# Performance work log

Measured on AMD Instinct MI355X. Metric: run time of the kernel, lower is better.

The kernel has to match this reference:

```python
import jax, jax.numpy as jnp
import numpy as np

EPS = 1e-8
SIM_THRESHOLD = 0.5


def _conv(x, src, dst, W, b):
    # Gather per-edge endpoint features: x_j = source, x_i = target (PyG default flow)
    x_j = x[src]
    x_i = x[dst]
    # Cosine similarity per edge
    dot = jnp.sum(x_i * x_j, axis=1)
    denom = jnp.maximum(jnp.linalg.norm(x_i, axis=1) * jnp.linalg.norm(x_j, axis=1), EPS)
    sim = dot / denom
    mask = (sim > SIM_THRESHOLD).astype(x.dtype)[:, None]
    msg = x_j * mask
    # Scatter-add aggregate into target nodes
    agg = jax.ops.segment_sum(msg, dst, num_segments=x.shape[0])
    # update: Linear
    return agg @ W.T + b


def setup_inputs() -> dict:
    key = jax.random.key(0)
    k1, k2, k3, k4, k5 = jax.random.split(key, 5)
    N, E, D_IN, D_HID, D_OUT = 50000, 800000, 128, 256, 64
    x = jax.random.normal(k1, (N, D_IN), dtype=jnp.float32)
    edge_index = jax.random.randint(k2, (2, E), 0, N, dtype=jnp.int64)
    # Xavier-uniform linear weights, zero-ish bias
    lim1 = float(np.sqrt(6.0 / (D_IN + D_HID)))
    lim2 = float(np.sqrt(6.0 / (D_HID + D_OUT)))
    W1 = jax.random.uniform(k3, (D_HID, D_IN), minval=-lim1, maxval=lim1, dtype=jnp.float32)
    b1 = jnp.zeros((D_HID,), dtype=jnp.float32)
    W2 = jax.random.uniform(k4, (D_OUT, D_HID), minval=-lim2, maxval=lim2, dtype=jnp.float32)
    b2 = jnp.zeros((D_OUT,), dtype=jnp.float32)
    return {"x": x, "edge_index": edge_index, "W1": W1, "b1": b1, "W2": W2, "b2": b2}


def reference(x, edge_index, W1, b1, W2, b2):
    N = x.shape[0]
    # add self-loops
    loops = jnp.arange(N, dtype=edge_index.dtype)
    src = jnp.concatenate([edge_index[0], loops])
    dst = jnp.concatenate([edge_index[1], loops])
    h = _conv(x, src, dst, W1, b1)
    h = jax.nn.relu(h)  # dropout is identity in eval mode
    out = _conv(h, src, dst, W2, b2)
    return jax.nn.log_softmax(out, axis=-1)
```

## Files before the change

kernel.cpp:

```cpp
#include <hip/hip_runtime.h>
#include <math.h>

#define EPS 1e-8f
#define NB_SORT 256

#if defined(__has_builtin)
#if __has_builtin(__builtin_amdgcn_sdot4)
#define HAVE_SDOT4 1
#endif
#endif

typedef __attribute__((ext_vector_type(8))) short bf16x8;
typedef __attribute__((ext_vector_type(4))) float f32x4;

__device__ __forceinline__ int sdot4i(int a, int b, int c) {
#ifdef HAVE_SDOT4
  return __builtin_amdgcn_sdot4(a, b, c, false);
#else
  return c + ((int)(signed char)(a)) * ((int)(signed char)(b)) +
         ((int)(signed char)(a >> 8)) * ((int)(signed char)(b >> 8)) +
         ((int)(signed char)(a >> 16)) * ((int)(signed char)(b >> 16)) +
         (a >> 24) * (b >> 24);
#endif
}

__device__ __forceinline__ float wave_reduce_sum(float v) {
#pragma unroll
  for (int off = 32; off > 0; off >>= 1)
    v += __shfl_xor(v, off, 64);
  return v;
}

__device__ __forceinline__ float wave_reduce_max(float v) {
#pragma unroll
  for (int off = 32; off > 0; off >>= 1)
    v = fmaxf(v, __shfl_xor(v, off, 64));
  return v;
}

__device__ __forceinline__ float dot4(float4 a, float4 b) {
  return a.x * b.x + a.y * b.y + a.z * b.z + a.w * b.w;
}

__device__ __forceinline__ int clampq(float q) {
  int i = (int)rintf(q);
  return i < -127 ? -127 : (i > 127 ? 127 : i);
}

__device__ __forceinline__ void split_bf16(float x, unsigned int& hi,
                                           unsigned int& lo) {
  unsigned int u = __float_as_uint(x);
  hi = u >> 16;
  float hf = __uint_as_float(u & 0xFFFF0000u);
  float r = x - hf;
  lo = __float_as_uint(r) >> 16;
}

__global__ __launch_bounds__(256) void hist_coarse(const int* __restrict__ dst,
                                                   int* __restrict__ hist_blk,
                                                   int E, int nbuck) {
  __shared__ int lh[1024];
  int t = threadIdx.x, blk = blockIdx.x;
  for (int i = t; i < nbuck; i += 256) lh[i] = 0;
  __syncthreads();
  int ch = (E + NB_SORT - 1) / NB_SORT;
  int lo = blk * ch, hi = min(E, lo + ch);
  for (int e = lo + t; e < hi; e += 256) atomicAdd(&lh[dst[e] >> 6], 1);
  __syncthreads();
  for (int i = t; i < nbuck; i += 256) hist_blk[i * NB_SORT + blk] = lh[i];
}

__global__ __launch_bounds__(256) void scan_local(int* __restrict__ hist,
                                                  int* __restrict__ bsum,
                                                  int nb) {
  __shared__ int tsum[256];
  int t = threadIdx.x;
  int base = blockIdx.x * 1024 + t * 4;
  int v0 = 0, v1 = 0, v2 = 0, v3 = 0;
  if (base + 3 < nb) {
    int4 q = *(const int4*)&hist[base];
    v0 = q.x; v1 = q.y; v2 = q.z; v3 = q.w;
  } else {
    if (base + 0 < nb) v0 = hist[base + 0];
    if (base + 1 < nb) v1 = hist[base + 1];
    if (base + 2 < nb) v2 = hist[base + 2];
  }
  tsum[t] = v0 + v1 + v2 + v3;
  __syncthreads();
  for (int off = 1; off < 256; off <<= 1) {
    int u = 0;
    if (t >= off) u = tsum[t - off];
    __syncthreads();
    if (t >= off) tsum[t] += u;
    __syncthreads();
  }
  int excl = (t == 0) ? 0 : tsum[t - 1];
  int e0 = excl, e1 = excl + v0, e2 = e1 + v1, e3 = e2 + v2;
  if (base + 3 < nb) {
    *(int4*)&hist[base] = make_int4(e0, e1, e2, e3);
  } else {
    if (base + 0 < nb) hist[base + 0] = e0;
    if (base + 1 < nb) hist[base + 1] = e1;
    if (base + 2 < nb) hist[base + 2] = e2;
  }
  if (t == 255) bsum[blockIdx.x] = tsum[255];
}

__global__ __launch_bounds__(256) void scan_bsum(int* __restrict__ bsum,
                                                 int nblk) {
  __shared__ int sh[256];
  int t = threadIdx.x;
  sh[t] = (t < nblk) ? bsum[t] : 0;
  __syncthreads();
  for (int off = 1; off < 256; off <<= 1) {
    int u = 0;
    if (t >= off) u = sh[t - off];
    __syncthreads();
    if (t >= off) sh[t] += u;
    __syncthreads();
  }
  if (t < nblk) bsum[t] = (t == 0) ? 0 : sh[t - 1];
}

__global__ __launch_bounds__(256) void add_bsum(int* __restrict__ hist,
                                                const int* __restrict__ bsum,
                                                int nb) {
  int i = blockIdx.x * blockDim.x + threadIdx.x;
  if (i < nb) hist[i] += bsum[i >> 10];
}

__global__ __launch_bounds__(256) void scatter_coarse(
    const int* __restrict__ src, const int* __restrict__ dst,
    const int* __restrict__ S, int2* __restrict__ epair, int E, int nbuck) {
  __shared__ int lb[1024];
  int t = threadIdx.x, blk = blockIdx.x;
  for (int i = t; i < nbuck; i += 256) lb[i] = S[i * NB_SORT + blk];
  __syncthreads();
  int ch = (E + NB_SORT - 1) / NB_SORT;
  int lo = blk * ch, hi = min(E, lo + ch);
  for (int e = lo + t; e < hi; e += 256) {
    int d = dst[e];
    int pos = atomicAdd(&lb[d >> 6], 1);
    epair[pos] = make_int2(src[e], d);
  }
}

__global__ __launch_bounds__(256) void fine_sort(
    const int2* __restrict__ epair, const int* __restrict__ S,
    int2* __restrict__ spair, int E, int nbuck) {
  __shared__ int fh[64];
  __shared__ int cur[64];
  int b = blockIdx.x, t = threadIdx.x;
  int bstart = S[b * NB_SORT];
  int bend = (b + 1 < nbuck) ? S[(b + 1) * NB_SORT] : E;
  if (t < 64) fh[t] = 0;
  __syncthreads();
  for (int e = bstart + t; e < bend; e += 256)
    atomicAdd(&fh[epair[e].y & 63], 1);
  __syncthreads();
  if (t < 64) {
    int v = fh[t];
    int incl = v;
#pragma unroll
    for (int off = 1; off < 64; off <<= 1) {
      int u = __shfl_up(incl, off, 64);
      if (t >= off) incl += u;
    }
    cur[t] = incl - v;
  }
  __syncthreads();
  for (int e = bstart + t; e < bend; e += 256) {
    int2 p = epair[e];
    int pos = atomicAdd(&cur[p.y & 63], 1);
    spair[bstart + pos] = p;
  }
}

__global__ __launch_bounds__(256) void prep_x(const float* __restrict__ x,
                                              signed char* __restrict__ qx,
                                              float4* __restrict__ nprop,
                                              float* __restrict__ agg,
                                              int N) {
  int node = (int)((blockIdx.x * blockDim.x + threadIdx.x) >> 6);
  int lane = threadIdx.x & 63;
  if (node >= N) return;
  float2 v = *(const float2*)(x + (size_t)node * 128 + lane * 2);
  float ax = fabsf(v.x), ay = fabsf(v.y);
  float mx = wave_reduce_max(fmaxf(ax, ay));
  float l1 = wave_reduce_sum(ax + ay);
  float ss = wave_reduce_sum(v.x * v.x + v.y * v.y);
  float s = mx * (1.0f / 127.0f);
  float inv = (mx > 0.f) ? 127.0f / mx : 0.f;
  int q0 = clampq(v.x * inv), q1 = clampq(v.y * inv);
  unsigned short w = (unsigned short)((q0 & 0xff) | ((q1 & 0xff) << 8));
  ((unsigned short*)(qx + (size_t)node * 128))[lane] = w;
  float l1q = s * wave_reduce_sum((float)(abs(q0) + abs(q1)));
  bool sp = ss > 0.5f * fmaxf(ss, EPS);
  *(float2*)(agg + (size_t)node * 128 + lane * 2) =
      sp ? v : make_float2(0.f, 0.f);
  if (lane == 0)
    nprop[node] = make_float4(sqrtf(ss), s, fmaxf(l1, l1q), 0.f);
}

__global__ __launch_bounds__(256) void prep_h(const float* __restrict__ h,
                                              signed char* __restrict__ qh,
                                              float4* __restrict__ nprop,
                                              float* __restrict__ agg,
                                              int N) {
  int node = (int)((blockIdx.x * blockDim.x + threadIdx.x) >> 6);
  int lane = threadIdx.x & 63;
  if (node >= N) return;
  float4 v = *(const float4*)(h + (size_t)node * 256 + lane * 4);
  float ax = fabsf(v.x), ay = fabsf(v.y), az = fabsf(v.z), aw = fabsf(v.w);
  float mx = wave_reduce_max(fmaxf(fmaxf(ax, ay), fmaxf(az, aw)));
  float l1 = wave_reduce_sum(ax + ay + az + aw);
  float ss = wave_reduce_sum(dot4(v, v));
  float s = mx * (1.0f / 127.0f);
  float inv = (mx > 0.f) ? 127.0f / mx : 0.f;
  int q0 = clampq(v.x * inv), q1 = clampq(v.y * inv);
  int q2 = clampq(v.z * inv), q3 = clampq(v.w * inv);
  int w = (q0 & 0xff) | ((q1 & 0xff) << 8) | ((q2 & 0xff) << 16) | (q3 << 24);
  ((int*)(qh + (size_t)node * 256))[lane] = w;
  float l1q = s * wave_reduce_sum((float)(abs(q0) + abs(q1) + abs(q2) + abs(q3)));
  bool sp = ss > 0.5f * fmaxf(ss, EPS);
  *(float4*)(agg + (size_t)node * 256 + lane * 4) =
      sp ? v : make_float4(0.f, 0.f, 0.f, 0.f);
  if (lane == 0)
    nprop[node] = make_float4(sqrtf(ss), s, fmaxf(l1, l1q), 0.f);
}

template <int D>
__global__ __launch_bounds__(256) void conv_coop(
    const float* __restrict__ xf, const signed char* __restrict__ qt,
    const float4* __restrict__ nprop, const int2* __restrict__ spair,
    float* __restrict__ agg, int E) {
  constexpr int G = D / 16;
  constexpr int EPW = 64 / G;
  constexpr int V = D / 64;
  const int tid = threadIdx.x;
  const int lane = tid & 63;
  const int wv = tid >> 6;
  const int g = lane & (G - 1);
  const int sub = lane / G;
  const int e = (blockIdx.x * 4 + wv) * EPW + sub;
  const bool valid = e < E;
  int2 p = spair[valid ? e : (E - 1)];
  const int s = p.x, d = p.y;
  float4 nps = nprop[s];
  float4 npd = nprop[d];
  int id = 0;
  {
    int4 a = *(const int4*)(qt + (size_t)s * D + g * 16);
    int4 bq = *(const int4*)(qt + (size_t)d * D + g * 16);
    id = sdot4i(a.x, bq.x, id);
    id = sdot4i(a.y, bq.y, id);
    id = sdot4i(a.z, bq.z, id);
    id = sdot4i(a.w, bq.w, id);
  }
#pragma unroll
  for (int off = G / 2; off > 0; off >>= 1) id += __shfl_xor(id, off, 64);
  float denom = fmaxf(nps.x * npd.x, EPS);
  float thr = 0.5f * denom;
  float approx = (nps.y * npd.y) * (float)id;
  float m = 0.5002f * (nps.y * npd.z + npd.y * nps.z) + 2e-6f * denom + 1e-7f;
  bool maybe = valid && (approx > thr - m);
  bool defp = maybe && (approx - m > thr);
  bool amb = maybe && !defp;
  unsigned long long defmask = __ballot(defp && g == 0);
  unsigned long long ambmask = __ballot(amb && g == 0);
  while (defmask) {
    int ln = __ffsll((long long)defmask) - 1;
    defmask &= defmask - 1;
    int es = __shfl(s, ln);
    int ed = __shfl(d, ln);
    float* arow = agg + (size_t)ed * D + lane * V;
    if constexpr (V == 2) {
      float2 a = *(const float2*)(xf + (size_t)es * D + lane * 2);
      atomicAdd(&arow[0], a.x);
      atomicAdd(&arow[1], a.y);
    } else {
      float4 a = *(const float4*)(xf + (size_t)es * D + lane * 4);
      atomicAdd(&arow[0], a.x);
      atomicAdd(&arow[1], a.y);
      atomicAdd(&arow[2], a.z);
      atomicAdd(&arow[3], a.w);
    }
  }
  while (ambmask) {
    int ln = __ffsll((long long)ambmask) - 1;
    ambmask &= ambmask - 1;
    int es = __shfl(s, ln);
    int ed = __shfl(d, ln);
    float nsx = __shfl(nps.x, ln);
    float ndx = __shfl(npd.x, ln);
    float sv[V], dvv[V];
    if constexpr (V == 2) {
      float2 a = *(const float2*)(xf + (size_t)es * D + lane * 2);
      float2 b = *(const float2*)(xf + (size_t)ed * D + lane * 2);
      sv[0] = a.x; sv[1] = a.y; dvv[0] = b.x; dvv[1] = b.y;
    } else {
      float4 a = *(const float4*)(xf + (size_t)es * D + lane * 4);
      float4 b = *(const float4*)(xf + (size_t)ed * D + lane * 4);
      sv[0] = a.x; sv[1] = a.y; sv[2] = a.z; sv[3] = a.w;
      dvv[0] = b.x; dvv[1] = b.y; dvv[2] = b.z; dvv[3] = b.w;
    }
    float dx = 0.f;
#pragma unroll
    for (int q = 0; q < V; ++q) dx += sv[q] * dvv[q];
    dx = wave_reduce_sum(dx);
    if (dx > 0.5f * fmaxf(nsx * ndx, EPS)) {
      float* arow = agg + (size_t)ed * D + lane * V;
#pragma unroll
      for (int q = 0; q < V; ++q) atomicAdd(&arow[q], sv[q]);
    }
  }
}

__global__ __launch_bounds__(256) void gemm1_mfma(
    const float* __restrict__ A, const float* __restrict__ W,
    const float* __restrict__ bias, float* __restrict__ C, int M) {
  constexpr int K = 128, NN = 256, BM = 128, BK = 32, PK = 40;
  __shared__ unsigned short Ah[BM * PK];
  __shared__ unsigned short Al[BM * PK];
  __shared__ unsigned short Wh[BM * PK];
  __shared__ unsigned short Wl[BM * PK];
  const int tid = threadIdx.x;
  const int m0 = blockIdx.x * BM;
  const int n0 = blockIdx.y * BM;
  const int lane = tid & 63;
  const int wv = tid >> 6;
  const int wr = wv >> 1, wc = wv & 1;
  const int lrow = lane & 15, kg = lane >> 4;
  f32x4 acc[4][4] = {};

  for (int k0 = 0; k0 < K; k0 += BK) {
#pragma unroll
    for (int i = 0; i < 4; ++i) {
      int f = tid + i * 256;
      int r = f >> 3, q = f & 7;
      int gm = m0 + r;
      float4 a = (gm < M) ? *(const float4*)&A[(size_t)gm * K + k0 + q * 4]
                          : make_float4(0.f, 0.f, 0.f, 0.f);
      float4 w = *(const float4*)&W[(size_t)(n0 + r) * K + k0 + q * 4];
      unsigned int h0, h1, h2, h3, l0, l1, l2, l3;
      split_bf16(a.x, h0, l0); split_bf16(a.y, h1, l1);
      split_bf16(a.z, h2, l2); split_bf16(a.w, h3, l3);
      *(uint2*)&Ah[r * PK + q * 4] =
          make_uint2(h0 | (h1 << 16), h2 | (h3 << 16));
      *(uint2*)&Al[r * PK + q * 4] =
          make_uint2(l0 | (l1 << 16), l2 | (l3 << 16));
      split_bf16(w.x, h0, l0); split_bf16(w.y, h1, l1);
      split_bf16(w.z, h2, l2); split_bf16(w.w, h3, l3);
      *(uint2*)&Wh[r * PK + q * 4] =
          make_uint2(h0 | (h1 << 16), h2 | (h3 << 16));
      *(uint2*)&Wl[r * PK + q * 4] =
          make_uint2(l0 | (l1 << 16), l2 | (l3 << 16));
    }
    __syncthreads();
    bf16x8 ah[4], al[4], bh[4], bl[4];
#pragma unroll
    for (int m = 0; m < 4; ++m) {
      int row = wr * 64 + m * 16 + lrow;
      ah[m] = *(const bf16x8*)&Ah[row * PK + kg * 8];
      al[m] = *(const bf16x8*)&Al[row * PK + kg * 8];
    }
#pragma unroll
    for (int n = 0; n < 4; ++n) {
      int row = wc * 64 + n * 16 + lrow;
      bh[n] = *(const bf16x8*)&Wh[row * PK + kg * 8];
      bl[n] = *(const bf16x8*)&Wl[row * PK + kg * 8];
    }
#pragma unroll
    for (int m = 0; m < 4; ++m)
#pragma unroll
      for (int n = 0; n < 4; ++n) {
        acc[m][n] = __builtin_amdgcn_mfma_f32_16x16x32_bf16(ah[m], bh[n],
                                                            acc[m][n], 0, 0, 0);
        acc[m][n] = __builtin_amdgcn_mfma_f32_16x16x32_bf16(ah[m], bl[n],
                                                            acc[m][n], 0, 0, 0);
        acc[m][n] = __builtin_amdgcn_mfma_f32_16x16x32_bf16(al[m], bh[n],
                                                            acc[m][n], 0, 0, 0);
      }
    __syncthreads();
  }

#pragma unroll
  for (int n = 0; n < 4; ++n) {
    int gc = n0 + wc * 64 + n * 16 + lrow;
    float bv = bias[gc];
#pragma unroll
    for (int m = 0; m < 4; ++m) {
      int gr0 = m0 + wr * 64 + m * 16 + kg * 4;
#pragma unroll
      for (int r = 0; r < 4; ++r) {
        int gm = gr0 + r;
        if (gm < M) {
          float v = acc[m][n][r] + bv;
          C[(size_t)gm * NN + gc] = fmaxf(v, 0.f);
        }
      }
    }
  }
}

__global__ __launch_bounds__(256) void split_w2(
    const float* __restrict__ W, unsigned short* __restrict__ Wh,
    unsigned short* __restrict__ Wl, int total4) {
  int i = blockIdx.x * 256 + threadIdx.x;
  if (i >= total4) return;
  float4 w = ((const float4*)W)[i];
  unsigned int h0, h1, h2, h3, l0, l1, l2, l3;
  split_bf16(w.x, h0, l0); split_bf16(w.y, h1, l1);
  split_bf16(w.z, h2, l2); split_bf16(w.w, h3, l3);
  ((uint2*)Wh)[i] = make_uint2(h0 | (h1 << 16), h2 | (h3 << 16));
  ((uint2*)Wl)[i] = make_uint2(l0 | (l1 << 16), l2 | (l3 << 16));
}

__global__ __launch_bounds__(256) void gemm2_mfma_lsm(
    const float* __restrict__ A, const unsigned short* __restrict__ Wh,
    const unsigned short* __restrict__ Wl, const float* __restrict__ bias,
    float* __restrict__ out, int M) {
  constexpr int K = 256;
  const int tid = threadIdx.x;
  const int lane = tid & 63;
  const int wv = tid >> 6;
  const int lrow = lane & 15, kg = lane >> 4;
  const int r0 = blockIdx.x * 128 + wv * 32;
  f32x4 acc[2][4] = {};

  for (int k0 = 0; k0 < K; k0 += 32) {
    bf16x8 ah[2], al[2];
#pragma unroll
    for (int m = 0; m < 2; ++m) {
      int row = r0 + m * 16 + lrow;
      const float* ap = A + (size_t)row * K + k0 + kg * 8;
      float4 a0 = *(const float4*)ap;
      float4 a1 = *(const float4*)(ap + 4);
      unsigned int hh[8], ll[8];
      split_bf16(a0.x, hh[0], ll[0]); split_bf16(a0.y, hh[1], ll[1]);
      split_bf16(a0.z, hh[2], ll[2]); split_bf16(a0.w, hh[3], ll[3]);
      split_bf16(a1.x, hh[4], ll[4]); split_bf16(a1.y, hh[5], ll[5]);
      split_bf16(a1.z, hh[6], ll[6]); split_bf16(a1.w, hh[7], ll[7]);
      bf16x8 th, tl;
#pragma unroll
      for (int j = 0; j < 8; ++j) {
        th[j] = (short)hh[j];
        tl[j] = (short)ll[j];
      }
      ah[m] = th;
      al[m] = tl;
    }
    bf16x8 bh[4], bl[4];
#pragma unroll
    for (int n = 0; n < 4; ++n) {
      int wrow = n * 16 + lrow;
      bh[n] = *(const bf16x8*)&Wh[(size_t)wrow * K + k0 + kg * 8];
      bl[n] = *(const bf16x8*)&Wl[(size_t)wrow * K + k0 + kg * 8];
    }
#pragma unroll
    for (int m = 0; m < 2; ++m)
#pragma unroll
      for (int n = 0; n < 4; ++n) {
        acc[m][n] = __builtin_amdgcn_mfma_f32_16x16x32_bf16(ah[m], bh[n],
                                                            acc[m][n], 0, 0, 0);
        acc[m][n] = __builtin_amdgcn_mfma_f32_16x16x32_bf16(ah[m], bl[n],
                                                            acc[m][n], 0, 0, 0);
        acc[m][n] = __builtin_amdgcn_mfma_f32_16x16x32_bf16(al[m], bh[n],
                                                            acc[m][n], 0, 0, 0);
      }
  }

  float bv[4];
#pragma unroll
  for (int n = 0; n < 4; ++n) bv[n] = bias[n * 16 + lrow];
#pragma unroll
  for (int m = 0; m < 2; ++m)
#pragma unroll
    for (int r = 0; r < 4; ++r) {
      int row = r0 + m * 16 + kg * 4 + r;
      float v[4];
      float mx = -1e30f;
#pragma unroll
      for (int n = 0; n < 4; ++n) {
        v[n] = acc[m][n][r] + bv[n];
        mx = fmaxf(mx, v[n]);
      }
#pragma unroll
      for (int off = 8; off > 0; off >>= 1)
        mx = fmaxf(mx, __shfl_xor(mx, off, 64));
      float s = 0.f;
#pragma unroll
      for (int n = 0; n < 4; ++n) s += expf(v[n] - mx);
#pragma unroll
      for (int off = 8; off > 0; off >>= 1) s += __shfl_xor(s, off, 64);
      float lg = logf(s);
      if (row < M) {
#pragma unroll
        for (int n = 0; n < 4; ++n)
          out[(size_t)row * 64 + n * 16 + lrow] = v[n] - mx - lg;
      }
    }
}

extern "C" void kernel_launch(void* const* d_in, const int* in_sizes, int n_in,
                              void* d_out, int out_size, void* d_ws,
                              size_t ws_size, hipStream_t stream) {
  const float* x  = (const float*)d_in[0];
  const int* eidx = (const int*)d_in[1];
  const float* W1 = (const float*)d_in[2];
  const float* b1 = (const float*)d_in[3];
  const float* W2 = (const float*)d_in[4];
  const float* b2 = (const float*)d_in[5];
  float* out = (float*)d_out;

  const int N = in_sizes[0] / 128;
  const int E = in_sizes[1] / 2;
  const int* src = eidx;
  const int* dst = eidx + E;

  const int nbuck = (N + 63) / 64;
  const int ntot = nbuck * NB_SORT;
  const int nblk2 = (ntot + 1023) / 1024;

  float* agg    = (float*)d_ws;
  float* h      = agg + (size_t)N * 256;
  float4* npx   = (float4*)(h + (size_t)N * 256);
  float4* nph   = npx + N;
  int* S        = (int*)(nph + N);
  int* bsum     = S + ntot;
  int2* spair   = (int2*)(bsum + 256);
  signed char* qh = (signed char*)(spair + E);
  unsigned short* W2h = (unsigned short*)(qh + (size_t)N * 256);
  unsigned short* W2l = W2h + 64 * 256;
  int2* epair   = (int2*)h;
  signed char* qx = (signed char*)(h + (size_t)N * 64);

  split_w2<<<16, 256, 0, stream>>>(W2, W2h, W2l, 64 * 256 / 4);

  hist_coarse<<<NB_SORT, 256, 0, stream>>>(dst, S, E, nbuck);
  scan_local<<<nblk2, 256, 0, stream>>>(S, bsum, ntot);
  scan_bsum<<<1, 256, 0, stream>>>(bsum, nblk2);
  add_bsum<<<(ntot + 255) / 256, 256, 0, stream>>>(S, bsum, ntot);
  scatter_coarse<<<NB_SORT, 256, 0, stream>>>(src, dst, S, epair, E, nbuck);
  fine_sort<<<nbuck, 256, 0, stream>>>(epair, S, spair, E, nbuck);

  prep_x<<<(N + 3) / 4, 256, 0, stream>>>(x, qx, npx, agg, N);
  conv_coop<128><<<(E + 31) / 32, 256, 0, stream>>>(x, qx, npx, spair, agg, E);
  gemm1_mfma<<<dim3((N + 127) / 128, 2), 256, 0, stream>>>(agg, W1, b1, h, N);

  prep_h<<<(N + 3) / 4, 256, 0, stream>>>(h, qh, nph, agg, N);
  conv_coop<256><<<(E + 15) / 16, 256, 0, stream>>>(h, qh, nph, spair, agg, E);
  gemm2_mfma_lsm<<<dim3((N + 127) / 128), 256, 0, stream>>>(agg, W2h, W2l, b2,
                                                            out, N);
}
```

Measured before the change: 275.5 us.

## Rewrite GEMM1 to read operands directly, pre-split W1, remap blocks per XCD

Replaces the LDS-staged 128x128-tile gemm1 with a register-direct kernel. Each wave loads its A rows from global memory and splits them to bf16 hi/lo in registers, and reads a pre-split bf16 W1 produced by a new split_w launch. Blocks are remapped so that consecutive workgroups land on the same XCD, which improves L2 sharing of A rows across the four column blocks. This removes LDS traffic and the __syncthreads barriers. In exchange, A is reloaded once per column block (four times instead of twice), there are more launches, and the A load has no row bound check (it relies on the padded workspace).

Measured after the change: 280.2 us. No clear change (+1.7%).

```diff
diff --git a/kernel.cpp b/kernel.cpp
--- a/kernel.cpp
+++ b/kernel.cpp
@@ -316,94 +316,7 @@
   }
 }
 
-__global__ __launch_bounds__(256) void gemm1_mfma(
-    const float* __restrict__ A, const float* __restrict__ W,
-    const float* __restrict__ bias, float* __restrict__ C, int M) {
-  constexpr int K = 128, NN = 256, BM = 128, BK = 32, PK = 40;
-  __shared__ unsigned short Ah[BM * PK];
-  __shared__ unsigned short Al[BM * PK];
-  __shared__ unsigned short Wh[BM * PK];
-  __shared__ unsigned short Wl[BM * PK];
-  const int tid = threadIdx.x;
-  const int m0 = blockIdx.x * BM;
-  const int n0 = blockIdx.y * BM;
-  const int lane = tid & 63;
-  const int wv = tid >> 6;
-  const int wr = wv >> 1, wc = wv & 1;
-  const int lrow = lane & 15, kg = lane >> 4;
-  f32x4 acc[4][4] = {};
-
-  for (int k0 = 0; k0 < K; k0 += BK) {
-#pragma unroll
-    for (int i = 0; i < 4; ++i) {
-      int f = tid + i * 256;
-      int r = f >> 3, q = f & 7;
-      int gm = m0 + r;
-      float4 a = (gm < M) ? *(const float4*)&A[(size_t)gm * K + k0 + q * 4]
-                          : make_float4(0.f, 0.f, 0.f, 0.f);
-      float4 w = *(const float4*)&W[(size_t)(n0 + r) * K + k0 + q * 4];
-      unsigned int h0, h1, h2, h3, l0, l1, l2, l3;
-      split_bf16(a.x, h0, l0); split_bf16(a.y, h1, l1);
-      split_bf16(a.z, h2, l2); split_bf16(a.w, h3, l3);
-      *(uint2*)&Ah[r * PK + q * 4] =
-          make_uint2(h0 | (h1 << 16), h2 | (h3 << 16));
-      *(uint2*)&Al[r * PK + q * 4] =
-          make_uint2(l0 | (l1 << 16), l2 | (l3 << 16));
-      split_bf16(w.x, h0, l0); split_bf16(w.y, h1, l1);
-      split_bf16(w.z, h2, l2); split_bf16(w.w, h3, l3);
-      *(uint2*)&Wh[r * PK + q * 4] =
-          make_uint2(h0 | (h1 << 16), h2 | (h3 << 16));
-      *(uint2*)&Wl[r * PK + q * 4] =
-          make_uint2(l0 | (l1 << 16), l2 | (l3 << 16));
-    }
-    __syncthreads();
-    bf16x8 ah[4], al[4], bh[4], bl[4];
-#pragma unroll
-    for (int m = 0; m < 4; ++m) {
-      int row = wr * 64 + m * 16 + lrow;
-      ah[m] = *(const bf16x8*)&Ah[row * PK + kg * 8];
-      al[m] = *(const bf16x8*)&Al[row * PK + kg * 8];
-    }
-#pragma unroll
-    for (int n = 0; n < 4; ++n) {
-      int row = wc * 64 + n * 16 + lrow;
-      bh[n] = *(const bf16x8*)&Wh[row * PK + kg * 8];
-      bl[n] = *(const bf16x8*)&Wl[row * PK + kg * 8];
-    }
-#pragma unroll
-    for (int m = 0; m < 4; ++m)
-#pragma unroll
-      for (int n = 0; n < 4; ++n) {
-        acc[m][n] = __builtin_amdgcn_mfma_f32_16x16x32_bf16(ah[m], bh[n],
-                                                            acc[m][n], 0, 0, 0);
-        acc[m][n] = __builtin_amdgcn_mfma_f32_16x16x32_bf16(ah[m], bl[n],
-                                                            acc[m][n], 0, 0, 0);
-        acc[m][n] = __builtin_amdgcn_mfma_f32_16x16x32_bf16(al[m], bh[n],
-                                                            acc[m][n], 0, 0, 0);
-      }
-    __syncthreads();
-  }
-
-#pragma unroll
-  for (int n = 0; n < 4; ++n) {
-    int gc = n0 + wc * 64 + n * 16 + lrow;
-    float bv = bias[gc];
-#pragma unroll
-    for (int m = 0; m < 4; ++m) {
-      int gr0 = m0 + wr * 64 + m * 16 + kg * 4;
-#pragma unroll
-      for (int r = 0; r < 4; ++r) {
-        int gm = gr0 + r;
-        if (gm < M) {
-          float v = acc[m][n][r] + bv;
-          C[(size_t)gm * NN + gc] = fmaxf(v, 0.f);
-        }
-      }
-    }
-  }
-}
-
-__global__ __launch_bounds__(256) void split_w2(
+__global__ __launch_bounds__(256) void split_w(
     const float* __restrict__ W, unsigned short* __restrict__ Wh,
     unsigned short* __restrict__ Wl, int total4) {
   int i = blockIdx.x * 256 + threadIdx.x;
@@ -414,6 +327,85 @@
   split_bf16(w.z, h2, l2); split_bf16(w.w, h3, l3);
   ((uint2*)Wh)[i] = make_uint2(h0 | (h1 << 16), h2 | (h3 << 16));
   ((uint2*)Wl)[i] = make_uint2(l0 | (l1 << 16), l2 | (l3 << 16));
+}
+
+__global__ __launch_bounds__(256) void gemm1_mfma2(
+    const float* __restrict__ A, const unsigned short* __restrict__ Wh,
+    const unsigned short* __restrict__ Wl, const float* __restrict__ bias,
+    float* __restrict__ C, int M, int nwg) {
+  constexpr int K = 128, NN = 256;
+  int orig = blockIdx.x;
+  int qq = nwg >> 3, rr8 = nwg & 7;
+  int xcd = orig & 7, loc = orig >> 3;
+  int wg = (xcd < rr8 ? xcd * (qq + 1) : rr8 * (qq + 1) + (xcd - rr8) * qq) + loc;
+  const int rowblk = wg >> 2, nblk = wg & 3;
+  const int tid = threadIdx.x;
+  const int lane = tid & 63;
+  const int wv = tid >> 6;
+  const int lrow = lane & 15, kg = lane >> 4;
+  const int r0 = rowblk * 128 + wv * 32;
+  const int n0 = nblk * 64;
+  f32x4 acc[2][4] = {};
+
+#pragma unroll
+  for (int k0 = 0; k0 < K; k0 += 32) {
+    bf16x8 ah[2], al[2];
+#pragma unroll
+    for (int m = 0; m < 2; ++m) {
+      int row = r0 + m * 16 + lrow;
+      const float* ap = A + (size_t)row * K + k0 + kg * 8;
+      float4 a0 = *(const float4*)ap;
+      float4 a1 = *(const float4*)(ap + 4);
+      unsigned int hh[8], ll[8];
+      split_bf16(a0.x, hh[0], ll[0]); split_bf16(a0.y, hh[1], ll[1]);
+      split_bf16(a0.z, hh[2], ll[2]); split_bf16(a0.w, hh[3], ll[3]);
+      split_bf16(a1.x, hh[4], ll[4]); split_bf16(a1.y, hh[5], ll[5]);
+      split_bf16(a1.z, hh[6], ll[6]); split_bf16(a1.w, hh[7], ll[7]);
+      bf16x8 th, tl;
+#pragma unroll
+      for (int j = 0; j < 8; ++j) {
+        th[j] = (short)hh[j];
+        tl[j] = (short)ll[j];
+      }
+      ah[m] = th;
+      al[m] = tl;
+    }
+    bf16x8 bh[4], bl[4];
+#pragma unroll
+    for (int n = 0; n < 4; ++n) {
+      int wrow = n0 + n * 16 + lrow;
+      bh[n] = *(const bf16x8*)&Wh[(size_t)wrow * K + k0 + kg * 8];
+      bl[n] = *(const bf16x8*)&Wl[(size_t)wrow * K + k0 + kg * 8];
+    }
+#pragma unroll
+    for (int m = 0; m < 2; ++m)
+#pragma unroll
+      for (int n = 0; n < 4; ++n) {
+        acc[m][n] = __builtin_amdgcn_mfma_f32_16x16x32_bf16(ah[m], bh[n],
+                                                            acc[m][n], 0, 0, 0);
+        acc[m][n] = __builtin_amdgcn_mfma_f32_16x16x32_bf16(ah[m], bl[n],
+                                                            acc[m][n], 0, 0, 0);
+        acc[m][n] = __builtin_amdgcn_mfma_f32_16x16x32_bf16(al[m], bh[n],
+                                                            acc[m][n], 0, 0, 0);
+      }
+  }
+
+  float bv[4];
+#pragma unroll
+  for (int n = 0; n < 4; ++n) bv[n] = bias[n0 + n * 16 + lrow];
+#pragma unroll
+  for (int m = 0; m < 2; ++m)
+#pragma unroll
+    for (int r = 0; r < 4; ++r) {
+      int row = r0 + m * 16 + kg * 4 + r;
+      if (row < M) {
+#pragma unroll
+        for (int n = 0; n < 4; ++n) {
+          float v = acc[m][n][r] + bv[n];
+          C[(size_t)row * NN + n0 + n * 16 + lrow] = fmaxf(v, 0.f);
+        }
+      }
+    }
 }
 
 __global__ __launch_bounds__(256) void gemm2_mfma_lsm(
@@ -532,10 +524,13 @@
   signed char* qh = (signed char*)(spair + E);
   unsigned short* W2h = (unsigned short*)(qh + (size_t)N * 256);
   unsigned short* W2l = W2h + 64 * 256;
+  unsigned short* W1h = W2l + 64 * 256;
+  unsigned short* W1l = W1h + 256 * 128;
   int2* epair   = (int2*)h;
   signed char* qx = (signed char*)(h + (size_t)N * 64);
 
-  split_w2<<<16, 256, 0, stream>>>(W2, W2h, W2l, 64 * 256 / 4);
+  split_w<<<16, 256, 0, stream>>>(W2, W2h, W2l, 64 * 256 / 4);
+  split_w<<<32, 256, 0, stream>>>(W1, W1h, W1l, 256 * 128 / 4);
 
   hist_coarse<<<NB_SORT, 256, 0, stream>>>(dst, S, E, nbuck);
   scan_local<<<nblk2, 256, 0, stream>>>(S, bsum, ntot);
@@ -546,7 +541,8 @@
 
   prep_x<<<(N + 3) / 4, 256, 0, stream>>>(x, qx, npx, agg, N);
   conv_coop<128><<<(E + 31) / 32, 256, 0, stream>>>(x, qx, npx, spair, agg, E);
-  gemm1_mfma<<<dim3((N + 127) / 128, 2), 256, 0, stream>>>(agg, W1, b1, h, N);
+  const int nwg1 = ((N + 127) / 128) * 4;
+  gemm1_mfma2<<<nwg1, 256, 0, stream>>>(agg, W1h, W1l, b1, h, N, nwg1);
 
   prep_h<<<(N + 3) / 4, 256, 0, stream>>>(h, qh, nph, agg, N);
   conv_coop<256><<<(E + 15) / 16, 256, 0, stream>>>(h, qh, nph, spair, agg, E);
```
